# Performance work log

Hardware: AMD Instinct MI355X
Metric: run time of the kernel (lower is better)

## Reference

```python
import jax, jax.numpy as jnp
import numpy as np

B, C_IN, IMG, P = 64, 3, 224, 16
GRID = IMG // P              # 14
N_PATCH = GRID * GRID        # 196
S = N_PATCH + 1              # 197 tokens incl CLS
D, H, HD = 768, 12, 64
DFF = 3072
L, PRUNE_AFTER = 12, 4
RATIO, EPS = 0.5, 1e-6
NEG = -1e30                  # additive mask value (softmax weight -> exactly 0 in fp32)
N_CLASSES = 1000
N_KEEP = max(1, int(S * (1.0 - RATIO)))  # 98, matches torch topk count


def _ln(x, g, b):
    m = x.mean(-1, keepdims=True)
    v = ((x - m) ** 2).mean(-1, keepdims=True)
    return (x - m) * jax.lax.rsqrt(v + EPS) * g + b


def _attn(x, qkv_w, qkv_b, proj_w, proj_b, amask):
    Bx, N, C = x.shape
    qkv = (x @ qkv_w.T + qkv_b).reshape(Bx, N, 3, H, HD).transpose(2, 0, 3, 1, 4)
    q, k, v = qkv[0], qkv[1], qkv[2]            # [B,H,N,HD]
    s = jnp.einsum('bhqd,bhkd->bhqk', q, k) * (HD ** -0.5)
    if amask is not None:
        s = s + amask                            # [B,1,1,N] broadcast
    a = jax.nn.softmax(s, axis=-1)
    o = jnp.einsum('bhqk,bhkd->bhqd', a, v).transpose(0, 2, 1, 3).reshape(Bx, N, C)
    return o @ proj_w.T + proj_b


def _block(x, i, p, amask=None):
    h = _ln(x, p['ln1_g'][i], p['ln1_b'][i])
    x = x + _attn(h, p['qkv_w'][i], p['qkv_b'][i], p['proj_w'][i], p['proj_b'][i], amask)
    h = _ln(x, p['ln2_g'][i], p['ln2_b'][i])
    h = jax.nn.gelu(h @ p['fc1_w'][i].T + p['fc1_b'][i], approximate=False)
    x = x + (h @ p['fc2_w'][i].T + p['fc2_b'][i])
    return x


def _forward(images, patch_w, patch_b, cls_token, pos_embed,
             ln1_g, ln1_b, qkv_w, qkv_b, proj_w, proj_b,
             ln2_g, ln2_b, fc1_w, fc1_b, fc2_w, fc2_b,
             norm_g, norm_b, head_w, head_b):
    p = dict(ln1_g=ln1_g, ln1_b=ln1_b, qkv_w=qkv_w, qkv_b=qkv_b,
             proj_w=proj_w, proj_b=proj_b, ln2_g=ln2_g, ln2_b=ln2_b,
             fc1_w=fc1_w, fc1_b=fc1_b, fc2_w=fc2_w, fc2_b=fc2_b)
    Bx = images.shape[0]
    # patch embed: non-overlapping 16x16 conv == patch extract + matmul
    patches = images.reshape(Bx, C_IN, GRID, P, GRID, P).transpose(0, 2, 4, 1, 3, 5)
    patches = patches.reshape(Bx, N_PATCH, C_IN * P * P)
    x = patches @ patch_w.reshape(D, -1).T + patch_b          # [B,196,768]
    x = jnp.concatenate([jnp.broadcast_to(cls_token, (Bx, 1, D)), x], axis=1)
    x = x + pos_embed                                          # [B,197,768]
    # early dense blocks
    for i in range(PRUNE_AFTER):
        x = _block(x, i, p)
    # _threshold_prune: topk on token norms, CLS always kept
    scores = jnp.linalg.norm(x, axis=-1)                       # [B,S]
    _, idx = jax.lax.top_k(scores, N_KEEP)                     # [B,98]
    mask = jnp.zeros((Bx, S), bool).at[jnp.arange(Bx)[:, None], idx].set(True)
    mask = mask.at[:, 0].set(True)
    # _gather_pad: kept tokens compacted to front (original order), zeros after
    order = jnp.argsort(~mask, axis=1, stable=True)            # True positions first
    x_pad = jnp.take_along_axis(x, order[:, :, None], axis=1)
    attn_m = jnp.take_along_axis(mask, order, axis=1)          # [B,S] True-prefix
    x_pad = x_pad * attn_m[:, :, None]
    amask = jnp.where(attn_m, 0.0, NEG).astype(x.dtype)[:, None, None, :]  # [B,1,1,S]
    # late masked blocks
    for i in range(PRUNE_AFTER, L):
        x_pad = _block(x_pad, i, p, amask)
    cls = _ln(x_pad[:, 0], norm_g, norm_b)
    return cls @ head_w.T + head_b                             # [B,1000]


def setup_inputs():
    key = jax.random.key(0)
    ks = iter(jax.random.split(key, 32))
    r = lambda shape: jax.random.normal(next(ks), shape, jnp.float32) * 0.02
    return {
        'images': jax.random.normal(next(ks), (B, C_IN, IMG, IMG), jnp.float32),
        'patch_w': r((D, C_IN, P, P)),
        'patch_b': r((D,)),
        'cls_token': r((1, 1, D)),
        'pos_embed': r((1, S, D)),
        'ln1_g': jnp.ones((L, D), jnp.float32),
        'ln1_b': jnp.zeros((L, D), jnp.float32),
        'qkv_w': r((L, 3 * D, D)),
        'qkv_b': r((L, 3 * D)),
        'proj_w': r((L, D, D)),
        'proj_b': r((L, D)),
        'ln2_g': jnp.ones((L, D), jnp.float32),
        'ln2_b': jnp.zeros((L, D), jnp.float32),
        'fc1_w': r((L, DFF, D)),
        'fc1_b': r((L, DFF)),
        'fc2_w': r((L, D, DFF)),
        'fc2_b': r((L, D)),
        'norm_g': jnp.ones((D,), jnp.float32),
        'norm_b': jnp.zeros((D,), jnp.float32),
        'head_w': r((N_CLASSES, D)),
        'head_b': r((N_CLASSES,)),
    }


def reference(images, patch_w, patch_b, cls_token, pos_embed,
              ln1_g, ln1_b, qkv_w, qkv_b, proj_w, proj_b,
              ln2_g, ln2_b, fc1_w, fc1_b, fc2_w, fc2_b,
              norm_g, norm_b, head_w, head_b):
    return _forward(images, patch_w, patch_b, cls_token, pos_embed,
                    ln1_g, ln1_b, qkv_w, qkv_b, proj_w, proj_b,
                    ln2_g, ln2_b, fc1_w, fc1_b, fc2_w, fc2_b,
                    norm_g, norm_b, head_w, head_b)
```

## Files before the change

### kernel.cpp

```cpp
#include <hip/hip_runtime.h>
#include <cstdint>
#include <cstddef>


#define NTOK 197
#define NB 64
#define NHEAD 12
#define SL 99

typedef __attribute__((ext_vector_type(8))) _Float16 half8;
typedef __attribute__((ext_vector_type(4))) float f32x4;
typedef __attribute__((ext_vector_type(4))) unsigned short us4;

#define DEV static __device__ __forceinline__

DEV unsigned short f2h(float f) {
    union { _Float16 h; unsigned short u; } v;
    v.h = (_Float16)f;
    return v.u;
}

DEV void gload16(const void* g, void* l) {
    __builtin_amdgcn_global_load_lds((const __attribute__((address_space(1))) unsigned int*)g,
                                     (__attribute__((address_space(3))) unsigned int*)l, 16, 0, 0);
}

__global__ __launch_bounds__(256) void cvt_layer_k(const float* __restrict__ qw,
                                                   const float* __restrict__ pw,
                                                   const float* __restrict__ f1,
                                                   const float* __restrict__ f2,
                                                   unsigned short* __restrict__ dh)
{
    size_t t = (size_t)blockIdx.x * 256 + threadIdx.x;
    size_t e = t * 4;
    const float* src; size_t loc;
    if (e < 1769472)      { src = qw; loc = e; }
    else if (e < 2359296) { src = pw; loc = e - 1769472; }
    else if (e < 4718592) { src = f1; loc = e - 2359296; }
    else                  { src = f2; loc = e - 4718592; }
    float4 v = *(const float4*)(src + loc);
    us4 hi; hi.x = f2h(v.x); hi.y = f2h(v.y); hi.z = f2h(v.z); hi.w = f2h(v.w);
    *(us4*)(dh + e) = hi;
}

__global__ __launch_bounds__(256) void cvt_simple_k(const float* __restrict__ src,
                                                    unsigned short* __restrict__ dh, int n4)
{
    int t = blockIdx.x * 256 + threadIdx.x;
    if (t >= n4) return;
    size_t e = (size_t)t * 4;
    float4 v = *(const float4*)(src + e);
    us4 hi; hi.x = f2h(v.x); hi.y = f2h(v.y); hi.z = f2h(v.z); hi.w = f2h(v.w);
    *(us4*)(dh + e) = hi;
}

__global__ __launch_bounds__(256) void patch_extract2_k(const float* __restrict__ img,
                                                        unsigned short* __restrict__ ph)
{
    int pi = blockIdx.x, b = blockIdx.y;
    int gy = pi / 14, gx = pi % 14;
    size_t obase = ((size_t)b * 196 + pi) * 768;
    for (int f = threadIdx.x; f < 768; f += 256) {
        int c = f >> 8, py = (f >> 4) & 15, px = f & 15;
        float v = img[(((size_t)b * 3 + c) * 224 + gy * 16 + py) * 224 + gx * 16 + px];
        ph[obase + f] = f2h(v);
    }
}

__global__ __launch_bounds__(256) void assemble_k(const float* __restrict__ emb,
                                                  const float* __restrict__ cls,
                                                  const float* __restrict__ pos,
                                                  float* __restrict__ x)
{
    int s = blockIdx.x, b = blockIdx.y;
    size_t xo = ((size_t)b * NTOK + s) * 768;
    for (int d = threadIdx.x; d < 768; d += 256) {
        float v = (s == 0) ? cls[d] : emb[((size_t)b * 196 + (s - 1)) * 768 + d];
        x[xo + d] = v + pos[(size_t)s * 768 + d];
    }
}

__global__ __launch_bounds__(256) void ln2_k(const float* __restrict__ in,
                                             unsigned short* __restrict__ outh,
                                             const float* __restrict__ g,
                                             const float* __restrict__ bt, size_t ldin)
{
    const float* xr = in + (size_t)blockIdx.x * ldin;
    size_t ob = (size_t)blockIdx.x * 768;
    int t = threadIdx.x;
    float v0 = xr[t], v1 = xr[t + 256], v2 = xr[t + 512];
    float s = v0 + v1 + v2;
#pragma unroll
    for (int o = 32; o; o >>= 1) s += __shfl_xor(s, o);
    __shared__ float r1[4], r2[4];
    int wv = t >> 6, ln = t & 63;
    if (ln == 0) r1[wv] = s;
    __syncthreads();
    float mean = (r1[0] + r1[1] + r1[2] + r1[3]) * (1.f / 768.f);
    float d0 = v0 - mean, d1 = v1 - mean, d2 = v2 - mean;
    float ss = d0 * d0 + d1 * d1 + d2 * d2;
#pragma unroll
    for (int o = 32; o; o >>= 1) ss += __shfl_xor(ss, o);
    if (ln == 0) r2[wv] = ss;
    __syncthreads();
    float inv = rsqrtf((r2[0] + r2[1] + r2[2] + r2[3]) * (1.f / 768.f) + 1e-6f);
    outh[ob + t]       = f2h(d0 * inv * g[t]       + bt[t]);
    outh[ob + t + 256] = f2h(d1 * inv * g[t + 256] + bt[t + 256]);
    outh[ob + t + 512] = f2h(d2 * inv * g[t + 512] + bt[t + 512]);
}

template<int EPI, int OS, int MAP>
__global__ __launch_bounds__(256) void mgemm_k(const unsigned short* __restrict__ Ah,
                                               const unsigned short* __restrict__ Wh,
                                               const float* __restrict__ bias,
                                               const float* __restrict__ res,
                                               unsigned short* __restrict__ Chi,
                                               float* __restrict__ Cf,
                                               int M, int N, int K, int nR, int nC, int nRmax)
{
    __shared__ unsigned short lds[2 * 8192];

    int rt, ct;
    {
        int bid = blockIdx.x;
        if (MAP == 0) { rt = bid % nR; ct = bid / nR; }
        else {
            int x = bid & 7, u = bid >> 3, rl, c;
            if (MAP == 2) { c = u % nC; rl = u / nC; }
            else          { rl = u % nRmax; c = u / nRmax; }
            rt = x + 8 * rl; ct = c;
            if (rt >= nR) return;
        }
    }
    const int row0 = rt << 7, col0 = ct << 7;
    const int tid = threadIdx.x;
    const int w = tid >> 6, lane = tid & 63;
    const int wr = w >> 1, wc = w & 1;
    const int srow = lane >> 2;
    const int schunk = ((lane & 3) ^ ((srow >> 1) & 3)) << 3;
    const int fr = lane & 15, fq = lane >> 4;
    const int rchunk = (fq ^ ((fr >> 1) & 3)) << 3;

    f32x4 acc[4][4];
#pragma unroll
    for (int m = 0; m < 4; m++)
#pragma unroll
        for (int n = 0; n < 4; n++) acc[m][n] = (f32x4)0.f;

    const int nk = K >> 5;

    auto stage = [&](int t, int bsel) {
        const int k0 = t << 5;
        unsigned short* Ad = lds + bsel * 8192;
        unsigned short* Bd = Ad + 4096;
#pragma unroll
        for (int i = 0; i < 2; i++) {
            int r = i * 64 + w * 16 + srow;
            int ga = row0 + r; if (ga > M - 1) ga = M - 1;
            int gb = col0 + r; if (gb > N - 1) gb = N - 1;
            gload16(Ah + (size_t)ga * K + k0 + schunk, Ad + i * 2048 + w * 512);
            gload16(Wh + (size_t)gb * K + k0 + schunk, Bd + i * 2048 + w * 512);
        }
    };

    stage(0, 0);
    stage(1, 1);
    for (int t = 0; t < nk; ++t) {
        const int bsel = t & 1;
        if (t + 1 < nk) asm volatile("s_waitcnt vmcnt(4)" ::: "memory");
        else            asm volatile("s_waitcnt vmcnt(0)" ::: "memory");
        __builtin_amdgcn_s_barrier();
        __builtin_amdgcn_sched_barrier(0);
        const unsigned short* Ab = lds + bsel * 8192;
        const unsigned short* Bb = Ab + 4096;
        half8 a[4], bb[4];
#pragma unroll
        for (int m = 0; m < 4; m++)
            a[m] = *(const half8*)(Ab + (wr * 64 + m * 16 + fr) * 32 + rchunk);
#pragma unroll
        for (int n = 0; n < 4; n++)
            bb[n] = *(const half8*)(Bb + (wc * 64 + n * 16 + fr) * 32 + rchunk);
        __builtin_amdgcn_sched_barrier(0);
        asm volatile("s_waitcnt lgkmcnt(0)" ::: "memory");
        __builtin_amdgcn_sched_barrier(0);
        __builtin_amdgcn_s_barrier();
        if (t + 2 < nk) stage(t + 2, bsel);
#pragma unroll
        for (int m = 0; m < 4; m++)
#pragma unroll
            for (int n = 0; n < 4; n++)
                acc[m][n] = __builtin_amdgcn_mfma_f32_16x16x32_f16(a[m], bb[n], acc[m][n], 0, 0, 0);
    }

#pragma unroll
    for (int m = 0; m < 4; m++) {
#pragma unroll
        for (int n = 0; n < 4; n++) {
            int col = col0 + wc * 64 + n * 16 + fr;
#pragma unroll
            for (int r = 0; r < 4; r++) {
                int row = row0 + wr * 64 + m * 16 + fq * 4 + r;
                if (row < M && col < N) {
                    float v = acc[m][n][r] + bias[col];
                    size_t o = (size_t)row * N + col;
                    if (EPI == 2) v += res[o];
                    if (EPI == 1) v = 0.5f * v * (1.f + erff(v * 0.70710678118654752f));
                    if (OS == 0) Cf[o] = v;
                    else Chi[o] = f2h(v);
                }
            }
        }
    }
}

template<int S, int KT, int PVKT, int PSTR>
__global__ __launch_bounds__(256) void attn2_k(const unsigned short* __restrict__ qh,
                                               unsigned short* __restrict__ oh,
                                               const int* __restrict__ cntp)
{
    constexpr int PVK = PVKT * 32;
    constexpr int QT = (S + 15) / 16;
    extern __shared__ unsigned short sh[];
    unsigned short* VT = sh;
    unsigned short* PL = sh + 64 * PSTR;

    const int h = blockIdx.x, b = blockIdx.y;
    const int tid = threadIdx.x, w = tid >> 6, lane = tid & 63;
    const int nk = cntp ? cntp[b] : S;
    const size_t qbase = (size_t)b * S * 2304 + (size_t)h * 64;
    const int fr = lane & 15, fq = lane >> 4;

    for (int j0 = 0; j0 < S; j0 += 32) {
        int j = j0 + (tid >> 3);
        int d8 = (tid & 7) * 8;
        if (j < S) {
            size_t src = qbase + (size_t)j * 2304 + 1536 + d8;
            us4 v0 = *(const us4*)(qh + src);
            us4 v1 = *(const us4*)(qh + src + 4);
            VT[(d8 + 0) * PSTR + j] = v0.x; VT[(d8 + 1) * PSTR + j] = v0.y;
            VT[(d8 + 2) * PSTR + j] = v0.z; VT[(d8 + 3) * PSTR + j] = v0.w;
            VT[(d8 + 4) * PSTR + j] = v1.x; VT[(d8 + 5) * PSTR + j] = v1.y;
            VT[(d8 + 6) * PSTR + j] = v1.z; VT[(d8 + 7) * PSTR + j] = v1.w;
        }
    }
    for (int idx = tid; idx < 64 * (PVK - S); idx += 256) {
        int d = idx / (PVK - S), j = S + idx % (PVK - S);
        VT[d * PSTR + j] = 0;
    }
    {
        unsigned short* Pw = PL + w * 16 * PSTR;
        for (int idx = lane; idx < 16 * (PVK - 16 * KT); idx += 64) {
            int rr = idx / (PVK - 16 * KT), cc = 16 * KT + idx % (PVK - 16 * KT);
            Pw[rr * PSTR + cc] = 0;
        }
    }
    __syncthreads();

    for (int qt = w; qt < QT; qt += 4) {
        int qr = qt * 16 + fr; int qrc = qr < S ? qr : S - 1;
        const size_t qrow = qbase + (size_t)qrc * 2304;
        half8 qf0[2];
#pragma unroll
        for (int ks = 0; ks < 2; ks++)
            qf0[ks] = *(const half8*)(qh + qrow + ks * 32 + fq * 8);
        f32x4 sc[KT];
#pragma unroll
        for (int kt = 0; kt < KT; kt++) {
            int ky = kt * 16 + fr; int kyc = ky < S ? ky : S - 1;
            const size_t krow = qbase + (size_t)kyc * 2304 + 768;
            f32x4 acc = (f32x4)0.f;
#pragma unroll
            for (int ks = 0; ks < 2; ks++) {
                half8 kh = *(const half8*)(qh + krow + ks * 32 + fq * 8);
                acc = __builtin_amdgcn_mfma_f32_16x16x32_f16(qf0[ks], kh, acc, 0, 0, 0);
            }
            sc[kt] = acc;
        }
        float mx[4] = {-3e38f, -3e38f, -3e38f, -3e38f};
#pragma unroll
        for (int kt = 0; kt < KT; kt++) {
            bool valid = (kt * 16 + fr) < nk;
#pragma unroll
            for (int r = 0; r < 4; r++) {
                float s = sc[kt][r] * 0.125f;
                sc[kt][r] = s;
                if (valid) mx[r] = fmaxf(mx[r], s);
            }
        }
#pragma unroll
        for (int off = 1; off < 16; off <<= 1)
#pragma unroll
            for (int r = 0; r < 4; r++) mx[r] = fmaxf(mx[r], __shfl_xor(mx[r], off));
        float sum[4] = {0.f, 0.f, 0.f, 0.f};
#pragma unroll
        for (int kt = 0; kt < KT; kt++) {
            bool valid = (kt * 16 + fr) < nk;
#pragma unroll
            for (int r = 0; r < 4; r++) {
                float p = valid ? __expf(sc[kt][r] - mx[r]) : 0.f;
                sc[kt][r] = p;
                sum[r] += p;
            }
        }
#pragma unroll
        for (int off = 1; off < 16; off <<= 1)
#pragma unroll
            for (int r = 0; r < 4; r++) sum[r] += __shfl_xor(sum[r], off);
        float inv[4];
#pragma unroll
        for (int r = 0; r < 4; r++) inv[r] = 1.f / sum[r];
        unsigned short* Pw = PL + w * 16 * PSTR;
#pragma unroll
        for (int kt = 0; kt < KT; kt++) {
#pragma unroll
            for (int r = 0; r < 4; r++)
                Pw[(fq * 4 + r) * PSTR + kt * 16 + fr] = f2h(sc[kt][r] * inv[r]);
        }
        f32x4 o[4];
#pragma unroll
        for (int n = 0; n < 4; n++) o[n] = (f32x4)0.f;
#pragma unroll
        for (int ks = 0; ks < PVKT; ks++) {
            half8 pa = *(const half8*)(Pw + fr * PSTR + ks * 32 + fq * 8);
#pragma unroll
            for (int n = 0; n < 4; n++) {
                half8 vb = *(const half8*)(VT + (n * 16 + fr) * PSTR + ks * 32 + fq * 8);
                o[n] = __builtin_amdgcn_mfma_f32_16x16x32_f16(pa, vb, o[n], 0, 0, 0);
            }
        }
#pragma unroll
        for (int n = 0; n < 4; n++) {
#pragma unroll
            for (int r = 0; r < 4; r++) {
                int row = qt * 16 + fq * 4 + r;
                if (row < S) {
                    size_t oidx = ((size_t)b * S + row) * 768 + (size_t)h * 64 + n * 16 + fr;
                    oh[oidx] = f2h(o[n][r]);
                }
            }
        }
    }
}

__global__ __launch_bounds__(256) void normsq_k(const float* __restrict__ x, float* __restrict__ norms)
{
    const float* xr = x + (size_t)blockIdx.x * 768;
    int t = threadIdx.x;
    float v0 = xr[t], v1 = xr[t + 256], v2 = xr[t + 512];
    float ss = v0 * v0 + v1 * v1 + v2 * v2;
#pragma unroll
    for (int o = 32; o; o >>= 1) ss += __shfl_xor(ss, o);
    __shared__ float r1[4];
    if ((t & 63) == 0) r1[t >> 6] = ss;
    __syncthreads();
    if (t == 0) norms[blockIdx.x] = r1[0] + r1[1] + r1[2] + r1[3];
}

__global__ __launch_bounds__(256) void topk_k(const float* __restrict__ norms,
                                              int* __restrict__ idxmap, int* __restrict__ cnt)
{
    int b = blockIdx.x, t = threadIdx.x;
    __shared__ float n[NTOK];
    __shared__ unsigned char kp[NTOK];
    if (t < NTOK) n[t] = norms[b * NTOK + t];
    __syncthreads();
    if (t < NTOK) {
        float me = n[t];
        int rank = 0;
        for (int j = 0; j < NTOK; j++) rank += (n[j] > me) || (n[j] == me && j < t);
        kp[t] = (rank < 98) || (t == 0);
    }
    __syncthreads();
    if (t == 0) {
        int c = 0;
        for (int s = 0; s < NTOK; s++) if (kp[s]) idxmap[b * SL + c++] = s;
        cnt[b] = c;
        for (int j = c; j < SL; j++) idxmap[b * SL + j] = 0;
    }
}

__global__ __launch_bounds__(256) void gather_k(const float* __restrict__ x, const int* __restrict__ idxmap,
                                                const int* __restrict__ cnt, float* __restrict__ xl)
{
    int j = blockIdx.x, b = blockIdx.y;
    size_t dst = ((size_t)b * SL + j) * 768;
    if (j < cnt[b]) {
        int s = idxmap[b * SL + j];
        size_t src = ((size_t)b * NTOK + s) * 768;
        for (int d = threadIdx.x; d < 768; d += 256) xl[dst + d] = x[src + d];
    } else {
        for (int d = threadIdx.x; d < 768; d += 256) xl[dst + d] = 0.f;
    }
}

extern "C" void kernel_launch(void* const* d_in, const int* in_sizes, int n_in,
                              void* d_out, int out_size, void* d_ws, size_t ws_size,
                              hipStream_t stream)
{
    const float* images  = (const float*)d_in[0];
    const float* patch_w = (const float*)d_in[1];
    const float* patch_b = (const float*)d_in[2];
    const float* cls_tok = (const float*)d_in[3];
    const float* pos_emb = (const float*)d_in[4];
    const float* ln1_g   = (const float*)d_in[5];
    const float* ln1_b   = (const float*)d_in[6];
    const float* qkv_w   = (const float*)d_in[7];
    const float* qkv_b   = (const float*)d_in[8];
    const float* proj_w  = (const float*)d_in[9];
    const float* proj_b  = (const float*)d_in[10];
    const float* ln2_g   = (const float*)d_in[11];
    const float* ln2_b   = (const float*)d_in[12];
    const float* fc1_w   = (const float*)d_in[13];
    const float* fc1_b   = (const float*)d_in[14];
    const float* fc2_w   = (const float*)d_in[15];
    const float* fc2_b   = (const float*)d_in[16];
    const float* norm_g  = (const float*)d_in[17];
    const float* norm_b  = (const float*)d_in[18];
    const float* head_w  = (const float*)d_in[19];
    const float* head_b  = (const float*)d_in[20];
    float* outp = (float*)d_out;

    char* W = (char*)d_ws;
    float* x = (float*)W;
    unsigned short* hbh = (unsigned short*)(W + 38731776);
    char* R = W + 77463552;
    unsigned short* wbh = (unsigned short*)(W + 232390656);
    unsigned short* pwh = (unsigned short*)(W + 260702208);
    unsigned short* hwb = (unsigned short*)(W + 263061504);
    float* norms = (float*)(W + 264634368);
    unsigned short* clsb = (unsigned short*)(W + 264684800);
    int* idxmap = (int*)(W + 264881408);
    int* cnt    = (int*)(W + 264906752);

    unsigned short* ph  = (unsigned short*)R;
    float* emb = (float*)(R + 38535168);
    unsigned short* qkh = (unsigned short*)R;
    unsigned short* ffh = (unsigned short*)R;
    float* xl = (float*)(R + 83886080);

    const int LDS_EARLY = (64 * 232 + 4 * 16 * 232) * 2;
    const int LDS_LATE  = (64 * 136 + 4 * 16 * 136) * 2;
    (void)hipFuncSetAttribute(reinterpret_cast<const void*>(&attn2_k<197, 13, 7, 232>),
                              hipFuncAttributeMaxDynamicSharedMemorySize, LDS_EARLY);
    (void)hipFuncSetAttribute(reinterpret_cast<const void*>(&attn2_k<99, 7, 4, 136>),
                              hipFuncAttributeMaxDynamicSharedMemorySize, LDS_LATE);

    const int nR1 = 99, nRm1 = 13;
    const int nRp = 98, nRmp = 13;
    const int nR2 = 50, nRm2 = 7;

    cvt_simple_k<<<576, 256, 0, stream>>>(patch_w, pwh, 147456);
    patch_extract2_k<<<dim3(196, NB), 256, 0, stream>>>(images, ph);
    mgemm_k<0, 0, 2><<<8 * nRmp * 6, 256, 0, stream>>>(ph, pwh, patch_b, nullptr,
        nullptr, emb, 12544, 768, 768, nRp, 6, nRmp);
    assemble_k<<<dim3(NTOK, NB), 256, 0, stream>>>(emb, cls_tok, pos_emb, x);

    const int M1 = NB * NTOK;
    for (int i = 0; i < 4; i++) {
        cvt_layer_k<<<6912, 256, 0, stream>>>(qkv_w + (size_t)i * 1769472, proj_w + (size_t)i * 589824,
                                              fc1_w + (size_t)i * 2359296, fc2_w + (size_t)i * 2359296,
                                              wbh);
        ln2_k<<<M1, 256, 0, stream>>>(x, hbh, ln1_g + (size_t)i * 768, ln1_b + (size_t)i * 768, 768);
        mgemm_k<0, 1, 1><<<8 * nRm1 * 18, 256, 0, stream>>>(hbh, wbh,
            qkv_b + (size_t)i * 2304, nullptr, qkh, nullptr, M1, 2304, 768, nR1, 18, nRm1);
        attn2_k<197, 13, 7, 232><<<dim3(NHEAD, NB), 256, LDS_EARLY, stream>>>(qkh, hbh, nullptr);
        mgemm_k<2, 0, 2><<<8 * nRm1 * 6, 256, 0, stream>>>(hbh, wbh + 1769472,
            proj_b + (size_t)i * 768, x, nullptr, x, M1, 768, 768, nR1, 6, nRm1);
        ln2_k<<<M1, 256, 0, stream>>>(x, hbh, ln2_g + (size_t)i * 768, ln2_b + (size_t)i * 768, 768);
        mgemm_k<1, 1, 1><<<8 * nRm1 * 24, 256, 0, stream>>>(hbh, wbh + 2359296,
            fc1_b + (size_t)i * 3072, nullptr, ffh, nullptr, M1, 3072, 768, nR1, 24, nRm1);
        mgemm_k<2, 0, 2><<<8 * nRm1 * 6, 256, 0, stream>>>(ffh, wbh + 4718592,
            fc2_b + (size_t)i * 768, x, nullptr, x, M1, 768, 3072, nR1, 6, nRm1);
    }

    normsq_k<<<M1, 256, 0, stream>>>(x, norms);
    topk_k<<<NB, 256, 0, stream>>>(norms, idxmap, cnt);
    gather_k<<<dim3(SL, NB), 256, 0, stream>>>(x, idxmap, cnt, xl);

    const int M2 = NB * SL;
    for (int i = 4; i < 12; i++) {
        cvt_layer_k<<<6912, 256, 0, stream>>>(qkv_w + (size_t)i * 1769472, proj_w + (size_t)i * 589824,
                                              fc1_w + (size_t)i * 2359296, fc2_w + (size_t)i * 2359296,
                                              wbh);
        ln2_k<<<M2, 256, 0, stream>>>(xl, hbh, ln1_g + (size_t)i * 768, ln1_b + (size_t)i * 768, 768);
        mgemm_k<0, 1, 1><<<8 * nRm2 * 18, 256, 0, stream>>>(hbh, wbh,
            qkv_b + (size_t)i * 2304, nullptr, qkh, nullptr, M2, 2304, 768, nR2, 18, nRm2);
        attn2_k<99, 7, 4, 136><<<dim3(NHEAD, NB), 256, LDS_LATE, stream>>>(qkh, hbh, cnt);
        mgemm_k<2, 0, 2><<<8 * nRm2 * 6, 256, 0, stream>>>(hbh, wbh + 1769472,
            proj_b + (size_t)i * 768, xl, nullptr, xl, M2, 768, 768, nR2, 6, nRm2);
        ln2_k<<<M2, 256, 0, stream>>>(xl, hbh, ln2_g + (size_t)i * 768, ln2_b + (size_t)i * 768, 768);
        mgemm_k<1, 1, 1><<<8 * nRm2 * 24, 256, 0, stream>>>(hbh, wbh + 2359296,
            fc1_b + (size_t)i * 3072, nullptr, ffh, nullptr, M2, 3072, 768, nR2, 24, nRm2);
        mgemm_k<2, 0, 2><<<8 * nRm2 * 6, 256, 0, stream>>>(ffh, wbh + 4718592,
            fc2_b + (size_t)i * 768, xl, nullptr, xl, M2, 768, 3072, nR2, 6, nRm2);
    }

    ln2_k<<<NB, 256, 0, stream>>>(xl, clsb, norm_g, norm_b, (size_t)SL * 768);
    cvt_simple_k<<<750, 256, 0, stream>>>(head_w, hwb, 192000);
    mgemm_k<0, 0, 0><<<8, 256, 0, stream>>>(clsb, hwb,
        head_b, nullptr, nullptr, outp, 64, 1000, 768, 1, 8, 1);
}
```

Measured before the change: 3.930 ms.

## Add 256x256-tile GEMM kernel with 4-stage LDS pipeline for QKV and FC1

Adds a new 512-thread GEMM kernel that computes 256x256 output tiles, using a 4-stage global-to-LDS async load ring and interleaved MFMA/stage scheduling with priority hints. It replaces the previous 128-row GEMM for the QKV and FC1 projections in both the full-length and pruned layers. The larger tile is meant to raise arithmetic intensity and cut the operand reloads from global memory. The cost is 128KB of LDS per block and fewer blocks, which may leave compute units idle or unevenly loaded, especially on the smaller pruned-token GEMMs.

Result: slower. 4.612 ms (+17.4%).

```diff
diff --git a/kernel.cpp b/kernel.cpp
--- a/kernel.cpp
+++ b/kernel.cpp
@@ -107,6 +107,137 @@
     outh[ob + t]       = f2h(d0 * inv * g[t]       + bt[t]);
     outh[ob + t + 256] = f2h(d1 * inv * g[t + 256] + bt[t + 256]);
     outh[ob + t + 512] = f2h(d2 * inv * g[t + 512] + bt[t + 512]);
+}
+
+template<int EPI, int OS>
+__global__ __launch_bounds__(512, 2) void gemm256_k(const unsigned short* __restrict__ Ah,
+                                                    const unsigned short* __restrict__ Wh,
+                                                    const float* __restrict__ bias,
+                                                    unsigned short* __restrict__ Chi,
+                                                    float* __restrict__ Cf,
+                                                    int M, int N, int K, int nR, int nC)
+{
+    extern __shared__ unsigned short lds[];
+
+    const int xcd = blockIdx.x & 7, u = blockIdx.x >> 3;
+    const int ct = u % nC, rl = u / nC;
+    const int rt = xcd + 8 * rl;
+    if (rt >= nR) return;
+    const int row0 = rt << 8, col0 = ct << 8;
+
+    const int tid = threadIdx.x;
+    const int w = tid >> 6, lane = tid & 63;
+    const int wr = w >> 2, wc = w & 3;
+    const int fr = lane & 15, fq = lane >> 4;
+    const int aoff = (fq ^ ((fr >> 1) & 3)) << 3;
+
+    const int nk = K >> 5;
+
+    const int srow = lane >> 2;
+    const int r0 = (w << 5) + srow;
+    const int r1 = r0 + 16;
+    const int cs = (((lane & 3) ^ ((srow >> 1) & 3)) << 3);
+    const int gA0 = (row0 + r0 < M) ? row0 + r0 : M - 1;
+    const int gA1 = (row0 + r1 < M) ? row0 + r1 : M - 1;
+    const int gB0 = (col0 + r0 < N) ? col0 + r0 : N - 1;
+    const int gB1 = (col0 + r1 < N) ? col0 + r1 : N - 1;
+
+    auto stageA = [&](int kt) {
+        const int k0 = kt << 5;
+        unsigned short* dst = lds + (kt & 3) * 16384 + ((w << 1) << 9);
+        gload16(Ah + (size_t)gA0 * K + k0 + cs, dst);
+        gload16(Ah + (size_t)gA1 * K + k0 + cs, dst + 512);
+    };
+    auto stageB = [&](int kt) {
+        const int k0 = kt << 5;
+        unsigned short* dst = lds + (kt & 3) * 16384 + 8192 + ((w << 1) << 9);
+        gload16(Wh + (size_t)gB0 * K + k0 + cs, dst);
+        gload16(Wh + (size_t)gB1 * K + k0 + cs, dst + 512);
+    };
+
+    f32x4 acc[8][4];
+#pragma unroll
+    for (int m = 0; m < 8; m++)
+#pragma unroll
+        for (int n = 0; n < 4; n++) acc[m][n] = (f32x4)0.f;
+
+    stageA(0); stageB(0);
+    if (nk > 1) { stageA(1); stageB(1); }
+    if (nk > 2) { stageA(2); stageB(2); }
+
+#define MF4(m, av) { \
+    acc[m][0] = __builtin_amdgcn_mfma_f32_16x16x32_f16(av, b0, acc[m][0], 0, 0, 0); \
+    acc[m][1] = __builtin_amdgcn_mfma_f32_16x16x32_f16(av, b1, acc[m][1], 0, 0, 0); \
+    acc[m][2] = __builtin_amdgcn_mfma_f32_16x16x32_f16(av, b2, acc[m][2], 0, 0, 0); \
+    acc[m][3] = __builtin_amdgcn_mfma_f32_16x16x32_f16(av, b3, acc[m][3], 0, 0, 0); }
+
+    for (int kt = 0; kt < nk; ++kt) {
+        if (kt + 2 < nk)      asm volatile("s_waitcnt vmcnt(8)" ::: "memory");
+        else if (kt + 1 < nk) asm volatile("s_waitcnt vmcnt(4)" ::: "memory");
+        else                  asm volatile("s_waitcnt vmcnt(0)" ::: "memory");
+        __builtin_amdgcn_s_barrier();
+        const unsigned short* sA = lds + (kt & 3) * 16384;
+        const unsigned short* sB = sA + 8192;
+
+        half8 b0 = *(const half8*)(sB + ((wc << 6) +  0 + fr) * 32 + aoff);
+        half8 b1 = *(const half8*)(sB + ((wc << 6) + 16 + fr) * 32 + aoff);
+        half8 b2 = *(const half8*)(sB + ((wc << 6) + 32 + fr) * 32 + aoff);
+        half8 b3 = *(const half8*)(sB + ((wc << 6) + 48 + fr) * 32 + aoff);
+        half8 a0 = *(const half8*)(sA + ((wr << 7) +   0 + fr) * 32 + aoff);
+        half8 a1 = *(const half8*)(sA + ((wr << 7) +  16 + fr) * 32 + aoff);
+        __builtin_amdgcn_sched_barrier(0);
+        if (kt + 3 < nk) stageA(kt + 3);
+        __builtin_amdgcn_sched_barrier(0);
+        half8 a2 = *(const half8*)(sA + ((wr << 7) +  32 + fr) * 32 + aoff);
+        half8 a3 = *(const half8*)(sA + ((wr << 7) +  48 + fr) * 32 + aoff);
+        __builtin_amdgcn_sched_barrier(0);
+        __builtin_amdgcn_s_setprio(1);
+        MF4(0, a0); MF4(1, a1);
+        __builtin_amdgcn_s_setprio(0);
+        __builtin_amdgcn_sched_barrier(0);
+        if (kt + 3 < nk) stageB(kt + 3);
+        __builtin_amdgcn_sched_barrier(0);
+        half8 a4 = *(const half8*)(sA + ((wr << 7) +  64 + fr) * 32 + aoff);
+        half8 a5 = *(const half8*)(sA + ((wr << 7) +  80 + fr) * 32 + aoff);
+        __builtin_amdgcn_sched_barrier(0);
+        __builtin_amdgcn_s_setprio(1);
+        MF4(2, a2); MF4(3, a3);
+        __builtin_amdgcn_s_setprio(0);
+        __builtin_amdgcn_sched_barrier(0);
+        half8 a6 = *(const half8*)(sA + ((wr << 7) +  96 + fr) * 32 + aoff);
+        half8 a7 = *(const half8*)(sA + ((wr << 7) + 112 + fr) * 32 + aoff);
+        __builtin_amdgcn_sched_barrier(0);
+        __builtin_amdgcn_s_setprio(1);
+        MF4(4, a4); MF4(5, a5);
+        __builtin_amdgcn_s_setprio(0);
+        __builtin_amdgcn_sched_barrier(0);
+        __builtin_amdgcn_s_setprio(1);
+        MF4(6, a6); MF4(7, a7);
+        __builtin_amdgcn_s_setprio(0);
+        asm volatile("s_waitcnt lgkmcnt(0)" ::: "memory");
+        __builtin_amdgcn_sched_barrier(0);
+    }
+#undef MF4
+
+#pragma unroll
+    for (int m = 0; m < 8; m++) {
+        const int rowb = row0 + (wr << 7) + (m << 4) + (fq << 2);
+#pragma unroll
+        for (int n = 0; n < 4; n++) {
+            const int col = col0 + (wc << 6) + (n << 4) + fr;
+            if (col >= N) continue;
+#pragma unroll
+            for (int r = 0; r < 4; r++) {
+                const int row = rowb + r;
+                if (row >= M) continue;
+                float v = acc[m][n][r] + bias[col];
+                size_t o = (size_t)row * N + col;
+                if (EPI == 1) v = 0.5f * v * (1.f + erff(v * 0.70710678118654752f));
+                if (OS == 0) Cf[o] = v;
+                else Chi[o] = f2h(v);
+            }
+        }
+    }
 }
 
 template<int EPI, int OS, int MAP>
@@ -440,14 +571,21 @@
 
     const int LDS_EARLY = (64 * 232 + 4 * 16 * 232) * 2;
     const int LDS_LATE  = (64 * 136 + 4 * 16 * 136) * 2;
+    const int LDS_G256  = 131072;
     (void)hipFuncSetAttribute(reinterpret_cast<const void*>(&attn2_k<197, 13, 7, 232>),
                               hipFuncAttributeMaxDynamicSharedMemorySize, LDS_EARLY);
     (void)hipFuncSetAttribute(reinterpret_cast<const void*>(&attn2_k<99, 7, 4, 136>),
                               hipFuncAttributeMaxDynamicSharedMemorySize, LDS_LATE);
+    (void)hipFuncSetAttribute(reinterpret_cast<const void*>(&gemm256_k<0, 1>),
+                              hipFuncAttributeMaxDynamicSharedMemorySize, LDS_G256);
+    (void)hipFuncSetAttribute(reinterpret_cast<const void*>(&gemm256_k<1, 1>),
+                              hipFuncAttributeMaxDynamicSharedMemorySize, LDS_G256);
 
     const int nR1 = 99, nRm1 = 13;
     const int nRp = 98, nRmp = 13;
     const int nR2 = 50, nRm2 = 7;
+    const int nR1q = 50, nR1qc = 7;
+    const int nR2q = 25, nR2qc = 4;
 
     cvt_simple_k<<<576, 256, 0, stream>>>(patch_w, pwh, 147456);
     patch_extract2_k<<<dim3(196, NB), 256, 0, stream>>>(images, ph);
@@ -461,14 +599,14 @@
                                               fc1_w + (size_t)i * 2359296, fc2_w + (size_t)i * 2359296,
                                               wbh);
         ln2_k<<<M1, 256, 0, stream>>>(x, hbh, ln1_g + (size_t)i * 768, ln1_b + (size_t)i * 768, 768);
-        mgemm_k<0, 1, 1><<<8 * nRm1 * 18, 256, 0, stream>>>(hbh, wbh,
-            qkv_b + (size_t)i * 2304, nullptr, qkh, nullptr, M1, 2304, 768, nR1, 18, nRm1);
+        gemm256_k<0, 1><<<8 * nR1qc * 9, 512, LDS_G256, stream>>>(hbh, wbh,
+            qkv_b + (size_t)i * 2304, qkh, nullptr, M1, 2304, 768, nR1q, 9);
         attn2_k<197, 13, 7, 232><<<dim3(NHEAD, NB), 256, LDS_EARLY, stream>>>(qkh, hbh, nullptr);
         mgemm_k<2, 0, 2><<<8 * nRm1 * 6, 256, 0, stream>>>(hbh, wbh + 1769472,
             proj_b + (size_t)i * 768, x, nullptr, x, M1, 768, 768, nR1, 6, nRm1);
         ln2_k<<<M1, 256, 0, stream>>>(x, hbh, ln2_g + (size_t)i * 768, ln2_b + (size_t)i * 768, 768);
-        mgemm_k<1, 1, 1><<<8 * nRm1 * 24, 256, 0, stream>>>(hbh, wbh + 2359296,
-            fc1_b + (size_t)i * 3072, nullptr, ffh, nullptr, M1, 3072, 768, nR1, 24, nRm1);
+        gemm256_k<1, 1><<<8 * nR1qc * 12, 512, LDS_G256, stream>>>(hbh, wbh + 2359296,
+            fc1_b + (size_t)i * 3072, ffh, nullptr, M1, 3072, 768, nR1q, 12);
         mgemm_k<2, 0, 2><<<8 * nRm1 * 6, 256, 0, stream>>>(ffh, wbh + 4718592,
             fc2_b + (size_t)i * 768, x, nullptr, x, M1, 768, 3072, nR1, 6, nRm1);
     }
@@ -483,14 +621,14 @@
                                               fc1_w + (size_t)i * 2359296, fc2_w + (size_t)i * 2359296,
                                               wbh);
         ln2_k<<<M2, 256, 0, stream>>>(xl, hbh, ln1_g + (size_t)i * 768, ln1_b + (size_t)i * 768, 768);
-        mgemm_k<0, 1, 1><<<8 * nRm2 * 18, 256, 0, stream>>>(hbh, wbh,
-            qkv_b + (size_t)i * 2304, nullptr, qkh, nullptr, M2, 2304, 768, nR2, 18, nRm2);
+        gemm256_k<0, 1><<<8 * nR2qc * 9, 512, LDS_G256, stream>>>(hbh, wbh,
+            qkv_b + (size_t)i * 2304, qkh, nullptr, M2, 2304, 768, nR2q, 9);
         attn2_k<99, 7, 4, 136><<<dim3(NHEAD, NB), 256, LDS_LATE, stream>>>(qkh, hbh, cnt);
         mgemm_k<2, 0, 2><<<8 * nRm2 * 6, 256, 0, stream>>>(hbh, wbh + 1769472,
             proj_b + (size_t)i * 768, xl, nullptr, xl, M2, 768, 768, nR2, 6, nRm2);
         ln2_k<<<M2, 256, 0, stream>>>(xl, hbh, ln2_g + (size_t)i * 768, ln2_b + (size_t)i * 768, 768);
-        mgemm_k<1, 1, 1><<<8 * nRm2 * 24, 256, 0, stream>>>(hbh, wbh + 2359296,
-            fc1_b + (size_t)i * 3072, nullptr, ffh, nullptr, M2, 3072, 768, nR2, 24, nRm2);
+        gemm256_k<1, 1><<<8 * nR2qc * 12, 512, LDS_G256, stream>>>(hbh, wbh + 2359296,
+            fc1_b + (size_t)i * 3072, ffh, nullptr, M2, 3072, 768, nR2q, 12);
         mgemm_k<2, 0, 2><<<8 * nRm2 * 6, 256, 0, stream>>>(ffh, wbh + 4718592,
             fc2_b + (size_t)i * 768, xl, nullptr, xl, M2, 768, 3072, nR2, 6, nRm2);
     }
```

## Store residual stream in fp16 and triple-buffer GEMM LDS pipeline

Applied to the files above, without the earlier changes.

The fp32 residual stream (x, xl, patch embedding output) becomes fp16 throughout, so layernorm, residual-add epilogues, normsq and gather read and write half the bytes. Separately, the GEMM main loop moves from two to three LDS buffers, issuing the next stage right after the barrier and dropping the second barrier and lgkmcnt wait per k-step. Together these cut memory traffic and sync stalls, at the cost of fp16 rounding accumulating in the residual across 12 layers and 50% more LDS per GEMM block, which can lower occupancy.

Measured after the change: 3.866 ms. No clear change (-1.6%).

```diff
diff --git a/kernel.cpp b/kernel.cpp
--- a/kernel.cpp
+++ b/kernel.cpp
@@ -18,6 +18,11 @@
     union { _Float16 h; unsigned short u; } v;
     v.h = (_Float16)f;
     return v.u;
+}
+DEV float h2f(unsigned short u) {
+    union { _Float16 h; unsigned short u; } v;
+    v.u = u;
+    return (float)v.h;
 }
 
 DEV void gload16(const void* g, void* l) {
@@ -67,28 +72,28 @@
     }
 }
 
-__global__ __launch_bounds__(256) void assemble_k(const float* __restrict__ emb,
+__global__ __launch_bounds__(256) void assemble_k(const unsigned short* __restrict__ emb,
                                                   const float* __restrict__ cls,
                                                   const float* __restrict__ pos,
-                                                  float* __restrict__ x)
+                                                  unsigned short* __restrict__ x)
 {
     int s = blockIdx.x, b = blockIdx.y;
     size_t xo = ((size_t)b * NTOK + s) * 768;
     for (int d = threadIdx.x; d < 768; d += 256) {
-        float v = (s == 0) ? cls[d] : emb[((size_t)b * 196 + (s - 1)) * 768 + d];
-        x[xo + d] = v + pos[(size_t)s * 768 + d];
-    }
-}
-
-__global__ __launch_bounds__(256) void ln2_k(const float* __restrict__ in,
+        float v = (s == 0) ? cls[d] : h2f(emb[((size_t)b * 196 + (s - 1)) * 768 + d]);
+        x[xo + d] = f2h(v + pos[(size_t)s * 768 + d]);
+    }
+}
+
+__global__ __launch_bounds__(256) void ln2_k(const unsigned short* __restrict__ in,
                                              unsigned short* __restrict__ outh,
                                              const float* __restrict__ g,
                                              const float* __restrict__ bt, size_t ldin)
 {
-    const float* xr = in + (size_t)blockIdx.x * ldin;
+    const unsigned short* xr = in + (size_t)blockIdx.x * ldin;
     size_t ob = (size_t)blockIdx.x * 768;
     int t = threadIdx.x;
-    float v0 = xr[t], v1 = xr[t + 256], v2 = xr[t + 512];
+    float v0 = h2f(xr[t]), v1 = h2f(xr[t + 256]), v2 = h2f(xr[t + 512]);
     float s = v0 + v1 + v2;
 #pragma unroll
     for (int o = 32; o; o >>= 1) s += __shfl_xor(s, o);
@@ -113,12 +118,12 @@
 __global__ __launch_bounds__(256) void mgemm_k(const unsigned short* __restrict__ Ah,
                                                const unsigned short* __restrict__ Wh,
                                                const float* __restrict__ bias,
-                                               const float* __restrict__ res,
+                                               const unsigned short* __restrict__ res,
                                                unsigned short* __restrict__ Chi,
                                                float* __restrict__ Cf,
                                                int M, int N, int K, int nR, int nC, int nRmax)
 {
-    __shared__ unsigned short lds[2 * 8192];
+    __shared__ unsigned short lds[3 * 8192];
 
     int rt, ct;
     {
@@ -149,9 +154,9 @@
 
     const int nk = K >> 5;
 
-    auto stage = [&](int t, int bsel) {
+    auto stage = [&](int t, int slot) {
         const int k0 = t << 5;
-        unsigned short* Ad = lds + bsel * 8192;
+        unsigned short* Ad = lds + slot * 8192;
         unsigned short* Bd = Ad + 4096;
 #pragma unroll
         for (int i = 0; i < 2; i++) {
@@ -165,13 +170,13 @@
 
     stage(0, 0);
     stage(1, 1);
+    int slot = 0, slot2 = 2;
     for (int t = 0; t < nk; ++t) {
-        const int bsel = t & 1;
         if (t + 1 < nk) asm volatile("s_waitcnt vmcnt(4)" ::: "memory");
         else            asm volatile("s_waitcnt vmcnt(0)" ::: "memory");
         __builtin_amdgcn_s_barrier();
-        __builtin_amdgcn_sched_barrier(0);
-        const unsigned short* Ab = lds + bsel * 8192;
+        if (t + 2 < nk) stage(t + 2, slot2);
+        const unsigned short* Ab = lds + slot * 8192;
         const unsigned short* Bb = Ab + 4096;
         half8 a[4], bb[4];
 #pragma unroll
@@ -180,16 +185,13 @@
 #pragma unroll
         for (int n = 0; n < 4; n++)
             bb[n] = *(const half8*)(Bb + (wc * 64 + n * 16 + fr) * 32 + rchunk);
-        __builtin_amdgcn_sched_barrier(0);
-        asm volatile("s_waitcnt lgkmcnt(0)" ::: "memory");
-        __builtin_amdgcn_sched_barrier(0);
-        __builtin_amdgcn_s_barrier();
-        if (t + 2 < nk) stage(t + 2, bsel);
 #pragma unroll
         for (int m = 0; m < 4; m++)
 #pragma unroll
             for (int n = 0; n < 4; n++)
                 acc[m][n] = __builtin_amdgcn_mfma_f32_16x16x32_f16(a[m], bb[n], acc[m][n], 0, 0, 0);
+        slot = (slot == 2) ? 0 : slot + 1;
+        slot2 = (slot2 == 2) ? 0 : slot2 + 1;
     }
 
 #pragma unroll
@@ -203,7 +205,7 @@
                 if (row < M && col < N) {
                     float v = acc[m][n][r] + bias[col];
                     size_t o = (size_t)row * N + col;
-                    if (EPI == 2) v += res[o];
+                    if (EPI == 2) v += h2f(res[o]);
                     if (EPI == 1) v = 0.5f * v * (1.f + erff(v * 0.70710678118654752f));
                     if (OS == 0) Cf[o] = v;
                     else Chi[o] = f2h(v);
@@ -342,11 +344,12 @@
     }
 }
 
-__global__ __launch_bounds__(256) void normsq_k(const float* __restrict__ x, float* __restrict__ norms)
-{
-    const float* xr = x + (size_t)blockIdx.x * 768;
+__global__ __launch_bounds__(256) void normsq_k(const unsigned short* __restrict__ x,
+                                                float* __restrict__ norms)
+{
+    const unsigned short* xr = x + (size_t)blockIdx.x * 768;
     int t = threadIdx.x;
-    float v0 = xr[t], v1 = xr[t + 256], v2 = xr[t + 512];
+    float v0 = h2f(xr[t]), v1 = h2f(xr[t + 256]), v2 = h2f(xr[t + 512]);
     float ss = v0 * v0 + v1 * v1 + v2 * v2;
 #pragma unroll
     for (int o = 32; o; o >>= 1) ss += __shfl_xor(ss, o);
@@ -379,8 +382,10 @@
     }
 }
 
-__global__ __launch_bounds__(256) void gather_k(const float* __restrict__ x, const int* __restrict__ idxmap,
-                                                const int* __restrict__ cnt, float* __restrict__ xl)
+__global__ __launch_bounds__(256) void gather_k(const unsigned short* __restrict__ x,
+                                                const int* __restrict__ idxmap,
+                                                const int* __restrict__ cnt,
+                                                unsigned short* __restrict__ xl)
 {
     int j = blockIdx.x, b = blockIdx.y;
     size_t dst = ((size_t)b * SL + j) * 768;
@@ -389,7 +394,7 @@
         size_t src = ((size_t)b * NTOK + s) * 768;
         for (int d = threadIdx.x; d < 768; d += 256) xl[dst + d] = x[src + d];
     } else {
-        for (int d = threadIdx.x; d < 768; d += 256) xl[dst + d] = 0.f;
+        for (int d = threadIdx.x; d < 768; d += 256) xl[dst + d] = 0;
     }
 }
 
@@ -421,22 +426,21 @@
     float* outp = (float*)d_out;
 
     char* W = (char*)d_ws;
-    float* x = (float*)W;
-    unsigned short* hbh = (unsigned short*)(W + 38731776);
-    char* R = W + 77463552;
-    unsigned short* wbh = (unsigned short*)(W + 232390656);
-    unsigned short* pwh = (unsigned short*)(W + 260702208);
-    unsigned short* hwb = (unsigned short*)(W + 263061504);
-    float* norms = (float*)(W + 264634368);
-    unsigned short* clsb = (unsigned short*)(W + 264684800);
-    int* idxmap = (int*)(W + 264881408);
-    int* cnt    = (int*)(W + 264906752);
-
-    unsigned short* ph  = (unsigned short*)R;
-    float* emb = (float*)(R + 38535168);
-    unsigned short* qkh = (unsigned short*)R;
-    unsigned short* ffh = (unsigned short*)R;
-    float* xl = (float*)(R + 83886080);
+    unsigned short* x16  = (unsigned short*)W;
+    unsigned short* hbh  = (unsigned short*)(W + 19365888);
+    char* R = W + 38731776;
+    unsigned short* ph   = (unsigned short*)R;
+    unsigned short* emb  = (unsigned short*)(R + 19365888);
+    unsigned short* qkh  = (unsigned short*)R;
+    unsigned short* ffh  = (unsigned short*)R;
+    unsigned short* xl16 = (unsigned short*)(W + 116195328);
+    unsigned short* wbh  = (unsigned short*)(W + 125927424);
+    unsigned short* pwh  = (unsigned short*)(W + 140083200);
+    unsigned short* hwb  = (unsigned short*)(W + 141262848);
+    float* norms         = (float*)(W + 142835712);
+    unsigned short* clsb = (unsigned short*)(W + 142886912);
+    int* idxmap          = (int*)(W + 142985216);
+    int* cnt             = (int*)(W + 143010560);
 
     const int LDS_EARLY = (64 * 232 + 4 * 16 * 232) * 2;
     const int LDS_LATE  = (64 * 136 + 4 * 16 * 136) * 2;
@@ -451,51 +455,51 @@
 
     cvt_simple_k<<<576, 256, 0, stream>>>(patch_w, pwh, 147456);
     patch_extract2_k<<<dim3(196, NB), 256, 0, stream>>>(images, ph);
-    mgemm_k<0, 0, 2><<<8 * nRmp * 6, 256, 0, stream>>>(ph, pwh, patch_b, nullptr,
-        nullptr, emb, 12544, 768, 768, nRp, 6, nRmp);
-    assemble_k<<<dim3(NTOK, NB), 256, 0, stream>>>(emb, cls_tok, pos_emb, x);
+    mgemm_k<0, 1, 2><<<8 * nRmp * 6, 256, 0, stream>>>(ph, pwh, patch_b, nullptr,
+        emb, nullptr, 12544, 768, 768, nRp, 6, nRmp);
+    assemble_k<<<dim3(NTOK, NB), 256, 0, stream>>>(emb, cls_tok, pos_emb, x16);
 
     const int M1 = NB * NTOK;
     for (int i = 0; i < 4; i++) {
         cvt_layer_k<<<6912, 256, 0, stream>>>(qkv_w + (size_t)i * 1769472, proj_w + (size_t)i * 589824,
                                               fc1_w + (size_t)i * 2359296, fc2_w + (size_t)i * 2359296,
                                               wbh);
-        ln2_k<<<M1, 256, 0, stream>>>(x, hbh, ln1_g + (size_t)i * 768, ln1_b + (size_t)i * 768, 768);
+        ln2_k<<<M1, 256, 0, stream>>>(x16, hbh, ln1_g + (size_t)i * 768, ln1_b + (size_t)i * 768, 768);
         mgemm_k<0, 1, 1><<<8 * nRm1 * 18, 256, 0, stream>>>(hbh, wbh,
             qkv_b + (size_t)i * 2304, nullptr, qkh, nullptr, M1, 2304, 768, nR1, 18, nRm1);
         attn2_k<197, 13, 7, 232><<<dim3(NHEAD, NB), 256, LDS_EARLY, stream>>>(qkh, hbh, nullptr);
-        mgemm_k<2, 0, 2><<<8 * nRm1 * 6, 256, 0, stream>>>(hbh, wbh + 1769472,
-            proj_b + (size_t)i * 768, x, nullptr, x, M1, 768, 768, nR1, 6, nRm1);
-        ln2_k<<<M1, 256, 0, stream>>>(x, hbh, ln2_g + (size_t)i * 768, ln2_b + (size_t)i * 768, 768);
+        mgemm_k<2, 1, 2><<<8 * nRm1 * 6, 256, 0, stream>>>(hbh, wbh + 1769472,
+            proj_b + (size_t)i * 768, x16, x16, nullptr, M1, 768, 768, nR1, 6, nRm1);
+        ln2_k<<<M1, 256, 0, stream>>>(x16, hbh, ln2_g + (size_t)i * 768, ln2_b + (size_t)i * 768, 768);
         mgemm_k<1, 1, 1><<<8 * nRm1 * 24, 256, 0, stream>>>(hbh, wbh + 2359296,
             fc1_b + (size_t)i * 3072, nullptr, ffh, nullptr, M1, 3072, 768, nR1, 24, nRm1);
-        mgemm_k<2, 0, 2><<<8 * nRm1 * 6, 256, 0, stream>>>(ffh, wbh + 4718592,
-            fc2_b + (size_t)i * 768, x, nullptr, x, M1, 768, 3072, nR1, 6, nRm1);
-    }
-
-    normsq_k<<<M1, 256, 0, stream>>>(x, norms);
+        mgemm_k<2, 1, 2><<<8 * nRm1 * 6, 256, 0, stream>>>(ffh, wbh + 4718592,
+            fc2_b + (size_t)i * 768, x16, x16, nullptr, M1, 768, 3072, nR1, 6, nRm1);
+    }
+
+    normsq_k<<<M1, 256, 0, stream>>>(x16, norms);
     topk_k<<<NB, 256, 0, stream>>>(norms, idxmap, cnt);
-    gather_k<<<dim3(SL, NB), 256, 0, stream>>>(x, idxmap, cnt, xl);
+    gather_k<<<dim3(SL, NB), 256, 0, stream>>>(x16, idxmap, cnt, xl16);
 
     const int M2 = NB * SL;
     for (int i = 4; i < 12; i++) {
         cvt_layer_k<<<6912, 256, 0, stream>>>(qkv_w + (size_t)i * 1769472, proj_w + (size_t)i * 589824,
                                               fc1_w + (size_t)i * 2359296, fc2_w + (size_t)i * 2359296,
                                               wbh);
-        ln2_k<<<M2, 256, 0, stream>>>(xl, hbh, ln1_g + (size_t)i * 768, ln1_b + (size_t)i * 768, 768);
+        ln2_k<<<M2, 256, 0, stream>>>(xl16, hbh, ln1_g + (size_t)i * 768, ln1_b + (size_t)i * 768, 768);
         mgemm_k<0, 1, 1><<<8 * nRm2 * 18, 256, 0, stream>>>(hbh, wbh,
             qkv_b + (size_t)i * 2304, nullptr, qkh, nullptr, M2, 2304, 768, nR2, 18, nRm2);
         attn2_k<99, 7, 4, 136><<<dim3(NHEAD, NB), 256, LDS_LATE, stream>>>(qkh, hbh, cnt);
-        mgemm_k<2, 0, 2><<<8 * nRm2 * 6, 256, 0, stream>>>(hbh, wbh + 1769472,
-            proj_b + (size_t)i * 768, xl, nullptr, xl, M2, 768, 768, nR2, 6, nRm2);
-        ln2_k<<<M2, 256, 0, stream>>>(xl, hbh, ln2_g + (size_t)i * 768, ln2_b + (size_t)i * 768, 768);
+        mgemm_k<2, 1, 2><<<8 * nRm2 * 6, 256, 0, stream>>>(hbh, wbh + 1769472,
+            proj_b + (size_t)i * 768, xl16, xl16, nullptr, M2, 768, 768, nR2, 6, nRm2);
+        ln2_k<<<M2, 256, 0, stream>>>(xl16, hbh, ln2_g + (size_t)i * 768, ln2_b + (size_t)i * 768, 768);
         mgemm_k<1, 1, 1><<<8 * nRm2 * 24, 256, 0, stream>>>(hbh, wbh + 2359296,
             fc1_b + (size_t)i * 3072, nullptr, ffh, nullptr, M2, 3072, 768, nR2, 24, nRm2);
-        mgemm_k<2, 0, 2><<<8 * nRm2 * 6, 256, 0, stream>>>(ffh, wbh + 4718592,
-            fc2_b + (size_t)i * 768, xl, nullptr, xl, M2, 768, 3072, nR2, 6, nRm2);
-    }
-
-    ln2_k<<<NB, 256, 0, stream>>>(xl, clsb, norm_g, norm_b, (size_t)SL * 768);
+        mgemm_k<2, 1, 2><<<8 * nRm2 * 6, 256, 0, stream>>>(ffh, wbh + 4718592,
+            fc2_b + (size_t)i * 768, xl16, xl16, nullptr, M2, 768, 3072, nR2, 6, nRm2);
+    }
+
+    ln2_k<<<NB, 256, 0, stream>>>(xl16, clsb, norm_g, norm_b, (size_t)SL * 768);
     cvt_simple_k<<<750, 256, 0, stream>>>(head_w, hwb, 192000);
     mgemm_k<0, 0, 0><<<8, 256, 0, stream>>>(clsb, hwb,
         head_b, nullptr, nullptr, outp, 64, 1000, 768, 1, 8, 1);
```
